# Performance work log

Measured on AMD Instinct MI355X. Metric: run time of the kernel, lower is better.

Reference implementation:

```python
import jax, jax.numpy as jnp
import numpy as np

BATCH = 1024
H = 1024  # input_size == hidden_size (forced by h0 = z.repeat)
STEPS = 4


def _uniform(key, shape, bound):
    return jax.random.uniform(key, shape, jnp.float32, -bound, bound)


def setup_inputs() -> dict:
    key = jax.random.key(0)
    ks = jax.random.split(key, 12)
    bound = 1.0 / np.sqrt(H)  # PyTorch LSTM/Linear default init range
    return {
        "z": jax.random.normal(ks[0], (BATCH, H), jnp.float32),
        # LSTM layer 0 (gate order: i, f, g, o)
        "W_ih0": _uniform(ks[1], (4 * H, H), bound),
        "W_hh0": _uniform(ks[2], (4 * H, H), bound),
        "b_ih0": _uniform(ks[3], (4 * H,), bound),
        "b_hh0": _uniform(ks[4], (4 * H,), bound),
        # LSTM layer 1
        "W_ih1": _uniform(ks[5], (4 * H, H), bound),
        "W_hh1": _uniform(ks[6], (4 * H, H), bound),
        "b_ih1": _uniform(ks[7], (4 * H,), bound),
        "b_hh1": _uniform(ks[8], (4 * H,), bound),
        # Output linear
        "W_lin": _uniform(ks[9], (H, H), bound),
        "b_lin": _uniform(ks[10], (H,), bound),
    }


def _lstm_cell(x, h, c, W_ih, W_hh, b_ih, b_hh):
    # PyTorch LSTM cell: gates = x W_ih^T + h W_hh^T + b_ih + b_hh, order i,f,g,o
    gates = x @ W_ih.T + h @ W_hh.T + (b_ih + b_hh)
    i, f, g, o = jnp.split(gates, 4, axis=-1)
    c_new = jax.nn.sigmoid(f) * c + jax.nn.sigmoid(i) * jnp.tanh(g)
    h_new = jax.nn.sigmoid(o) * jnp.tanh(c_new)
    return h_new, c_new


def reference(z, W_ih0, W_hh0, b_ih0, b_hh0, W_ih1, W_hh1, b_ih1, b_hh1, W_lin, b_lin):
    # init_hidden: both layers' h and c start as z; input each step is the constant z
    def step(carry, _):
        h0, c0, h1, c1 = carry
        h0, c0 = _lstm_cell(z, h0, c0, W_ih0, W_hh0, b_ih0, b_hh0)
        h1, c1 = _lstm_cell(h0, h1, c1, W_ih1, W_hh1, b_ih1, b_hh1)
        return (h0, c0, h1, c1), h1

    init = (z, z, z, z)
    _, outs = jax.lax.scan(step, init, None, length=STEPS)  # [4, B, H]
    feat = jnp.transpose(outs, (1, 0, 2))  # [B, 4, H]
    return feat @ W_lin.T + b_lin
```

## Files before the change

kernel.cpp:

```cpp
#include <hip/hip_runtime.h>
#include <hip/hip_bf16.h>
#include <cstdint>
#include <cstddef>


typedef __bf16 bf16_t;
typedef __bf16 bf16x8 __attribute__((ext_vector_type(8)));
typedef __bf16 bf16x4 __attribute__((ext_vector_type(4)));
typedef float f32x4 __attribute__((ext_vector_type(4)));

__device__ __forceinline__ void gload_lds16(const bf16_t* g, bf16_t* l) {
    __builtin_amdgcn_global_load_lds(
        (const __attribute__((address_space(1))) void*)g,
        (__attribute__((address_space(3))) void*)l,
        16, 0, 0);
}

__device__ __forceinline__ float sigmoid_f(float x) {
    return 1.f / (1.f + __expf(-x));
}
__device__ __forceinline__ float tanh_fast(float x) {
    const float t = __expf(2.f * x);
    return 1.f - 2.f / (t + 1.f);
}

struct Job {
    const bf16_t* A;
    const bf16_t* B;
    const float*  add;
    const float*  bias;
    float*        c;
    bf16_t*       h1;
    bf16_t*       h2;
    float*        C;
    int lda, K, h1s, h2s, mode;
};

__global__ __launch_bounds__(256, 3) void fused_multi(Job j0, Job j1, Job j2, int n0, int n01)
{
    __shared__ __align__(16) char smem[32768];
    bf16_t* lsA = (bf16_t*)smem;
    bf16_t* lsB = (bf16_t*)(smem + 16384);
    float*  gsm = (float*)smem;

    const int bid = blockIdx.x;
    Job ja; int local, n;
    if (bid < n0)        { ja = j0; local = bid;       n = n0; }
    else if (bid < n01)  { ja = j1; local = bid - n0;  n = n01 - n0; }
    else                 { ja = j2; local = bid - n01; n = (int)gridDim.x - n01; }

    const int q    = n >> 3;
    const int tile = (local & 7) * q + (local >> 3);
    const int bcol = (tile >> 3) * 128;
    const int brow = (tile & 7) * 128;

    const int tid  = threadIdx.x;
    const int lane = tid & 63;
    const int wave = tid >> 6;
    const int wm = (wave >> 1) * 64;
    const int wn = (wave & 1) * 64;

    const int srow = lane >> 3;
    const int ssw  = ((lane & 7) ^ srow) * 8;
    const int ch0  = wave * 4;
    const int nkt  = ja.K >> 6;

    const int fr  = lane & 15;
    const int g8  = (lane >> 4) * 8;
    const int rsw = (fr & 7) * 8;

    f32x4 acc[4][4] = {};

    for (int kt = 0; kt < nkt; ++kt) {
        const int ktel = kt << 6;
#pragma unroll
        for (int it = 0; it < 4; ++it) {
            const int ch = ch0 + it;
            const int row = ch * 8 + srow;
            gload_lds16(ja.A + (size_t)(brow + row) * ja.lda + ktel + ssw, &lsA[ch * 512]);
            gload_lds16(ja.B + (size_t)(bcol + row) * ja.K   + ktel + ssw, &lsB[ch * 512]);
        }
        __syncthreads();
#pragma unroll
        for (int kk = 0; kk < 2; ++kk) {
            const int ko = (kk * 32 + g8) ^ rsw;
            bf16x8 af[4], bfv[4];
#pragma unroll
            for (int m = 0; m < 4; ++m)
                af[m] = *(const bf16x8*)&lsA[(wm + m * 16 + fr) * 64 + ko];
#pragma unroll
            for (int nn = 0; nn < 4; ++nn)
                bfv[nn] = *(const bf16x8*)&lsB[(wn + nn * 16 + fr) * 64 + ko];
#pragma unroll
            for (int m = 0; m < 4; ++m)
#pragma unroll
                for (int nn = 0; nn < 4; ++nn)
                    acc[m][nn] = __builtin_amdgcn_mfma_f32_16x16x32_bf16(af[m], bfv[nn], acc[m][nn], 0, 0, 0);
        }
        __syncthreads();
    }

    const int cr = (lane >> 4) * 4;
    const int cc = lane & 15;

    if (ja.mode == 1) {
#pragma unroll
        for (int nn = 0; nn < 4; ++nn) {
            const int col = bcol + wn + nn * 16 + cc;
            const float bv = ja.bias ? ja.bias[col] : 0.f;
#pragma unroll
            for (int m = 0; m < 4; ++m) {
                const int row0 = brow + wm + m * 16 + cr;
#pragma unroll
                for (int r = 0; r < 4; ++r)
                    ja.C[(size_t)(row0 + r) * 4096 + col] = acc[m][nn][r] + bv;
            }
        }
        return;
    }

#pragma unroll
    for (int h = 0; h < 2; ++h) {
        if ((wave & 1) == h) {
#pragma unroll
            for (int nn = 0; nn < 4; ++nn)
#pragma unroll
                for (int m = 0; m < 4; ++m)
#pragma unroll
                    for (int r = 0; r < 4; ++r)
                        gsm[(wm + m * 16 + cr + r) * 64 + nn * 16 + cc] = acc[m][nn][r];
        }
        __syncthreads();
#pragma unroll
        for (int p = 0; p < 8; ++p) {
            const int idx = p * 256 + tid;
            const int rl = idx >> 4;
            const int nn = idx & 15;
            float4 gv = *(const float4*)&gsm[rl * 64 + nn * 4];
            const int grow = brow + rl;
            const int j0c = bcol + h * 64 + nn * 4;
            if (ja.add) {
                const float4 av = *(const float4*)&ja.add[(size_t)grow * 4096 + j0c];
                gv.x += av.x; gv.y += av.y; gv.z += av.z; gv.w += av.w;
            }
            if (ja.bias) {
                const float4 bv = *(const float4*)&ja.bias[j0c];
                gv.x += bv.x; gv.y += bv.y; gv.z += bv.z; gv.w += bv.w;
            }
            const int ng = j0c >> 2;
            const size_t ci = (size_t)grow * 1024 + ng;
            const float cn = sigmoid_f(gv.y) * ja.c[ci] + sigmoid_f(gv.x) * tanh_fast(gv.z);
            const float hh = sigmoid_f(gv.w) * tanh_fast(cn);
            ja.c[ci] = cn;
            const bf16_t hb = (bf16_t)hh;
            ja.h1[(size_t)grow * ja.h1s + ng] = hb;
            if (ja.h2) ja.h2[(size_t)grow * ja.h2s + ng] = hb;
        }
        __syncthreads();
    }
}

__global__ __launch_bounds__(256) void prep_all(
    const float* __restrict__ z,
    const float4* __restrict__ Wih0, const float4* __restrict__ Whh0,
    const float4* __restrict__ Wih1, const float4* __restrict__ Whh1,
    const float4* __restrict__ Wlin,
    const float* __restrict__ bih0, const float* __restrict__ bhh0,
    const float* __restrict__ bih1, const float* __restrict__ bhh1,
    bf16x4* __restrict__ Wih0R, bf16x4* __restrict__ Whh0R, bf16x4* __restrict__ Wsum0R,
    bf16x4* __restrict__ WcatR1, bf16x4* __restrict__ Wlinb,
    bf16_t* __restrict__ zb, bf16_t* __restrict__ X0,
    float* __restrict__ c0, float* __restrict__ c1,
    float* __restrict__ b0R, float* __restrict__ b1R)
{
    const int t = blockIdx.x * 256 + threadIdx.x;
    if (t < 1048576) {
        const int j = t >> 8, col = t & 255;
        const int g = j & 3, nn = j >> 2;
        const int src = (g * 1024 + nn) * 256 + col;
        const float4 a = Wih0[src];
        const float4 b = Whh0[src];
        bf16x4 va = {(bf16_t)a.x, (bf16_t)a.y, (bf16_t)a.z, (bf16_t)a.w};
        bf16x4 vb = {(bf16_t)b.x, (bf16_t)b.y, (bf16_t)b.z, (bf16_t)b.w};
        bf16x4 vs = {(bf16_t)(a.x + b.x), (bf16_t)(a.y + b.y),
                     (bf16_t)(a.z + b.z), (bf16_t)(a.w + b.w)};
        Wih0R[t] = va; Whh0R[t] = vb; Wsum0R[t] = vs;
    } else if (t < 2097152) {
        const int i = t - 1048576;
        const int j = i >> 8, col = i & 255;
        const int g = j & 3, nn = j >> 2;
        const int src = (g * 1024 + nn) * 256 + col;
        const float4 a = Wih1[src];
        const float4 b = Whh1[src];
        bf16x4 va = {(bf16_t)a.x, (bf16_t)a.y, (bf16_t)a.z, (bf16_t)a.w};
        bf16x4 vb = {(bf16_t)b.x, (bf16_t)b.y, (bf16_t)b.z, (bf16_t)b.w};
        WcatR1[j * 512 + col]       = va;
        WcatR1[j * 512 + 256 + col] = vb;
    } else if (t < 2359296) {
        const int i = t - 2097152;
        const float4 a = Wlin[i];
        bf16x4 v = {(bf16_t)a.x, (bf16_t)a.y, (bf16_t)a.z, (bf16_t)a.w};
        Wlinb[i] = v;
    } else if (t < 2621440) {
        const int i = t - 2359296;
        const int b = i >> 8, n4 = i & 255;
        const float4 v = ((const float4*)z)[i];
        bf16x4 hv = {(bf16_t)v.x, (bf16_t)v.y, (bf16_t)v.z, (bf16_t)v.w};
        ((bf16x4*)zb)[i] = hv;
        *(bf16x4*)(X0 + (size_t)b * 2048 + 1024 + n4 * 4) = hv;
        ((float4*)c0)[i] = v;
        ((float4*)c1)[i] = v;
    } else if (t < 2622464) {
        const int nn = t - 2621440;
        float4 b0, b1;
        float* p0 = (float*)&b0; float* p1 = (float*)&b1;
#pragma unroll
        for (int g = 0; g < 4; ++g) {
            p0[g] = bih0[g * 1024 + nn] + bhh0[g * 1024 + nn];
            p1[g] = bih1[g * 1024 + nn] + bhh1[g * 1024 + nn];
        }
        ((float4*)b0R)[nn] = b0;
        ((float4*)b1R)[nn] = b1;
    }
}

extern "C" void kernel_launch(void* const* d_in, const int* in_sizes, int n_in,
                              void* d_out, int out_size, void* d_ws, size_t ws_size,
                              hipStream_t stream)
{
    const float* z     = (const float*)d_in[0];
    const float* W_ih0 = (const float*)d_in[1];
    const float* W_hh0 = (const float*)d_in[2];
    const float* b_ih0 = (const float*)d_in[3];
    const float* b_hh0 = (const float*)d_in[4];
    const float* W_ih1 = (const float*)d_in[5];
    const float* W_hh1 = (const float*)d_in[6];
    const float* b_ih1 = (const float*)d_in[7];
    const float* b_hh1 = (const float*)d_in[8];
    const float* W_lin = (const float*)d_in[9];
    const float* b_lin = (const float*)d_in[10];
    float* out = (float*)d_out;

    char* ws = (char*)d_ws;
    const size_t MB = 1u << 20;
    bf16_t* WcatR1 = (bf16_t*)(ws);
    bf16_t* Whh0R  = (bf16_t*)(ws + 16 * MB);
    bf16_t* Wih0R  = (bf16_t*)(ws + 24 * MB);
    bf16_t* Wsum0R = (bf16_t*)(ws + 32 * MB);
    bf16_t* Wlinb  = (bf16_t*)(ws + 40 * MB);
    bf16_t* zb     = (bf16_t*)(ws + 42 * MB);
    bf16_t* Xbuf   = (bf16_t*)(ws + 44 * MB);
    float*  Gz0R   = (float*) (ws + 52 * MB);
    bf16_t* stash  = (bf16_t*)(ws + 68 * MB);
    float*  c0     = (float*) (ws + 76 * MB);
    float*  c1     = (float*) (ws + 80 * MB);
    float*  bias0R = (float*) (ws + 84 * MB);
    float*  bias1R = (float*) (ws + 84 * MB + 16384);
    bf16_t* X[2] = {Xbuf, Xbuf + (size_t)(1u << 21)};

    prep_all<<<10244, 256, 0, stream>>>(
        z, (const float4*)W_ih0, (const float4*)W_hh0,
        (const float4*)W_ih1, (const float4*)W_hh1, (const float4*)W_lin,
        b_ih0, b_hh0, b_ih1, b_hh1,
        (bf16x4*)Wih0R, (bf16x4*)Whh0R, (bf16x4*)Wsum0R,
        (bf16x4*)WcatR1, (bf16x4*)Wlinb,
        zb, X[0], c0, c1, bias0R, bias1R);

    Job empty = {};

    {
        Job gz = {};
        gz.A = zb; gz.lda = 1024; gz.B = Wih0R; gz.K = 1024;
        gz.bias = bias0R; gz.C = Gz0R; gz.mode = 1;
        Job f00 = {};
        f00.A = zb; f00.lda = 1024; f00.B = Wsum0R; f00.K = 1024;
        f00.bias = bias0R; f00.c = c0; f00.h1 = X[0]; f00.h1s = 2048; f00.mode = 0;
        fused_multi<<<512, 256, 0, stream>>>(gz, f00, empty, 256, 512);
    }

    for (int t = 0; t < 4; ++t) {
        const int p = t & 1;
        Job a0 = {};
        a0.A = X[p]; a0.lda = 2048; a0.B = WcatR1; a0.K = 2048;
        a0.bias = bias1R; a0.c = c1;
        a0.h1 = stash + (size_t)t * (1u << 20); a0.h1s = 1024;
        if (t < 3) { a0.h2 = X[p ^ 1] + 1024; a0.h2s = 2048; }
        a0.mode = 0;

        Job a1 = {};
        if (t < 3) {
            a1.A = X[p]; a1.lda = 2048; a1.B = Whh0R; a1.K = 1024;
            a1.add = Gz0R; a1.c = c0; a1.h1 = X[p ^ 1]; a1.h1s = 2048; a1.mode = 0;
        }

        Job lj = {};
        if (t >= 1) {
            lj.A = stash + (size_t)(t - 1) * (1u << 20); lj.lda = 1024;
            lj.B = Wlinb; lj.K = 1024; lj.bias = b_lin;
            lj.C = out + (size_t)(t - 1) * 1024; lj.mode = 1;
        }

        if (t == 0)      fused_multi<<<512, 256, 0, stream>>>(a0, a1, empty, 256, 512);
        else if (t < 3)  fused_multi<<<576, 256, 0, stream>>>(a0, a1, lj, 256, 512);
        else             fused_multi<<<320, 256, 0, stream>>>(a0, lj, empty, 256, 320);
    }

    {
        Job lj = {};
        lj.A = stash + (size_t)3 * (1u << 20); lj.lda = 1024;
        lj.B = Wlinb; lj.K = 1024; lj.bias = b_lin;
        lj.C = out + (size_t)3 * 1024; lj.mode = 1;
        fused_multi<<<64, 256, 0, stream>>>(lj, empty, empty, 64, 64);
    }
}
```

Baseline: 247.0 us.

## Double-buffer LDS staging with K-tile of 32 and swizzle epilogue scratch

Shrinks the K tile from 64 to 32 and splits the 32KB shared buffer into two halves, so the next tile's global-to-LDS load is issued before the current tile's MFMAs run. This drops one barrier per iteration and overlaps memory with compute. The input swizzle is removed, which may add LDS bank conflicts on fragment reads. The epilogue scratch gets an XOR swizzle against bank conflicts, and launch bounds go from 3 to 4 blocks per CU, which may raise register pressure.

```diff
diff --git a/kernel.cpp b/kernel.cpp
--- a/kernel.cpp
+++ b/kernel.cpp
@@ -36,12 +36,9 @@
     int lda, K, h1s, h2s, mode;
 };
 
-__global__ __launch_bounds__(256, 3) void fused_multi(Job j0, Job j1, Job j2, int n0, int n01)
+__global__ __launch_bounds__(256, 4) void fused_multi(Job j0, Job j1, Job j2, int n0, int n01)
 {
     __shared__ __align__(16) char smem[32768];
-    bf16_t* lsA = (bf16_t*)smem;
-    bf16_t* lsB = (bf16_t*)(smem + 16384);
-    float*  gsm = (float*)smem;
 
     const int bid = blockIdx.x;
     Job ja; int local, n;
@@ -60,43 +57,49 @@
     const int wm = (wave >> 1) * 64;
     const int wn = (wave & 1) * 64;
 
-    const int srow = lane >> 3;
-    const int ssw  = ((lane & 7) ^ srow) * 8;
-    const int ch0  = wave * 4;
-    const int nkt  = ja.K >> 6;
-
-    const int fr  = lane & 15;
-    const int g8  = (lane >> 4) * 8;
-    const int rsw = (fr & 7) * 8;
+    const int srow = lane >> 2;
+    const int scol = (lane & 3) * 8;
+    const int nkt  = ja.K >> 5;
+
+    const int fr   = lane & 15;
+    const int s0k  = (lane >> 4) * 8;
+    const int aoff = (wm + fr) * 32 + s0k;
+    const int boff = (wn + fr) * 32 + s0k;
 
     f32x4 acc[4][4] = {};
 
+    auto stage = [&](int buf, int ktel) {
+        bf16_t* lsA = (bf16_t*)(smem + buf * 16384);
+        bf16_t* lsB = (bf16_t*)(smem + buf * 16384 + 8192);
+#pragma unroll
+        for (int it = 0; it < 2; ++it) {
+            const int ch = wave * 2 + it;
+            const int row = ch * 16 + srow;
+            gload_lds16(ja.A + (size_t)(brow + row) * ja.lda + ktel + scol, &lsA[ch * 512]);
+            gload_lds16(ja.B + (size_t)(bcol + row) * ja.K   + ktel + scol, &lsB[ch * 512]);
+        }
+    };
+
+    stage(0, 0);
+    __syncthreads();
+
     for (int kt = 0; kt < nkt; ++kt) {
-        const int ktel = kt << 6;
-#pragma unroll
-        for (int it = 0; it < 4; ++it) {
-            const int ch = ch0 + it;
-            const int row = ch * 8 + srow;
-            gload_lds16(ja.A + (size_t)(brow + row) * ja.lda + ktel + ssw, &lsA[ch * 512]);
-            gload_lds16(ja.B + (size_t)(bcol + row) * ja.K   + ktel + ssw, &lsB[ch * 512]);
-        }
-        __syncthreads();
-#pragma unroll
-        for (int kk = 0; kk < 2; ++kk) {
-            const int ko = (kk * 32 + g8) ^ rsw;
-            bf16x8 af[4], bfv[4];
-#pragma unroll
-            for (int m = 0; m < 4; ++m)
-                af[m] = *(const bf16x8*)&lsA[(wm + m * 16 + fr) * 64 + ko];
+        const int buf = kt & 1;
+        if (kt + 1 < nkt) stage(buf ^ 1, (kt + 1) << 5);
+        const bf16_t* lsA = (const bf16_t*)(smem + buf * 16384);
+        const bf16_t* lsB = (const bf16_t*)(smem + buf * 16384 + 8192);
+        bf16x8 af[4], bfv[4];
+#pragma unroll
+        for (int m = 0; m < 4; ++m)
+            af[m] = *(const bf16x8*)&lsA[aoff + m * 512];
+#pragma unroll
+        for (int nn = 0; nn < 4; ++nn)
+            bfv[nn] = *(const bf16x8*)&lsB[boff + nn * 512];
+#pragma unroll
+        for (int m = 0; m < 4; ++m)
 #pragma unroll
             for (int nn = 0; nn < 4; ++nn)
-                bfv[nn] = *(const bf16x8*)&lsB[(wn + nn * 16 + fr) * 64 + ko];
-#pragma unroll
-            for (int m = 0; m < 4; ++m)
-#pragma unroll
-                for (int nn = 0; nn < 4; ++nn)
-                    acc[m][nn] = __builtin_amdgcn_mfma_f32_16x16x32_bf16(af[m], bfv[nn], acc[m][nn], 0, 0, 0);
-        }
+                acc[m][nn] = __builtin_amdgcn_mfma_f32_16x16x32_bf16(af[m], bfv[nn], acc[m][nn], 0, 0, 0);
         __syncthreads();
     }
 
@@ -119,6 +122,7 @@
         return;
     }
 
+    float* gsm = (float*)smem;
 #pragma unroll
     for (int h = 0; h < 2; ++h) {
         if ((wave & 1) == h) {
@@ -127,8 +131,11 @@
 #pragma unroll
                 for (int m = 0; m < 4; ++m)
 #pragma unroll
-                    for (int r = 0; r < 4; ++r)
-                        gsm[(wm + m * 16 + cr + r) * 64 + nn * 16 + cc] = acc[m][nn][r];
+                    for (int r = 0; r < 4; ++r) {
+                        const int row = wm + m * 16 + cr + r;
+                        const int col = nn * 16 + cc;
+                        gsm[row * 64 + (col ^ (((row >> 2) & 1) << 4))] = acc[m][nn][r];
+                    }
         }
         __syncthreads();
 #pragma unroll
@@ -136,7 +143,7 @@
             const int idx = p * 256 + tid;
             const int rl = idx >> 4;
             const int nn = idx & 15;
-            float4 gv = *(const float4*)&gsm[rl * 64 + nn * 4];
+            float4 gv = *(const float4*)&gsm[rl * 64 + ((nn * 4) ^ (((rl >> 2) & 1) << 4))];
             const int grow = brow + rl;
             const int j0c = bcol + h * 64 + nn * 4;
             if (ja.add) {
```

After: 287.7 us. 16.4% more time.
